# Kernel tuning notes

Hardware: AMD Instinct MI355X
Metric: run time of the kernel (lower is better)

Reference implementation:

```python
import jax, jax.numpy as jnp
import numpy as np

SIGMA = 0.248
PRNUM = 6
P = 7.5
K = 3.0
ALPHA = 2.5


def _gauss_kernel():
    # 5x5 normalized Gaussian, replicated per channel for depthwise conv [O=3,I=1,5,5]
    x = jnp.arange(-2, 3, dtype=jnp.float32)
    x2, y2 = jnp.meshgrid(x, x, indexing='xy')
    k = jnp.exp(-(x2 ** 2 + y2 ** 2) / (2.0 * SIGMA ** 2))
    k = k / jnp.sum(k)
    return jnp.broadcast_to(k[None, None], (3, 1, 5, 5))


def _dwconv(x, k):
    # x: [3,H,W]; depthwise 5x5 conv, padding=2 (matches F.conv2d(..., padding=2, groups=3))
    return jax.lax.conv_general_dilated(
        x[None], k, window_strides=(1, 1), padding=[(2, 2), (2, 2)],
        feature_group_count=3, dimension_numbers=('NCHW', 'OIHW', 'NCHW'))[0]


def _down2(x):
    # torch bilinear align_corners=False at exact scale 0.5 == 2x2 average pooling
    c, h, w = x.shape
    return x.reshape(c, h // 2, 2, w // 2, 2).mean(axis=(2, 4))


def _up(x, hw):
    # torch bilinear align_corners=False upsample (half-pixel centers) == jax linear resize
    return jax.image.resize(x, (x.shape[0], hw[0], hw[1]), method='linear')


def _foveate(img, fixs):
    C, H, W = img.shape
    k = _gauss_kernel()
    # build Gaussian pyramid
    G = img
    pyr = [G]
    for _ in range(1, PRNUM):
        G = _down2(_dwconv(G, k))
        pyr.append(G)
    # re-expand each level back to full res (interpolate then blur at each step)
    As = [pyr[0]]
    for i in range(1, PRNUM):
        cur = pyr[i]
        for j in range(i):
            hw = (cur.shape[1] * 2, cur.shape[2] * 2) if j < i - 1 else (H, W)
            cur = _dwconv(_up(cur, hw), k)
        As.append(cur)
    As = jnp.stack(As)  # [prNum, 3, H, W]

    # radial eccentricity map (min distance over fixations)
    x = jnp.arange(W, dtype=jnp.float32)
    y = jnp.arange(H, dtype=jnp.float32)
    x2d, y2d = jnp.meshgrid(x, y, indexing='xy')  # each [H, W]
    d = jnp.sqrt((x2d[None] - fixs[:, 0, None, None]) ** 2 +
                 (y2d[None] - fixs[:, 1, None, None]) ** 2) / P
    theta = jnp.min(d, axis=0)
    R = ALPHA / (theta + ALPHA)

    Ts = [jnp.exp(-((2.0 ** (i - 3)) * R / SIGMA) ** 2 * K) for i in range(1, PRNUM)]
    Ts.append(jnp.zeros_like(R))

    om = np.minimum(np.sqrt(np.log(2.0) / K) / (2.0 ** np.arange(-2, 3)) * SIGMA, 1.0)
    omega = np.concatenate([om, [0.0]]).astype(np.float32)  # [prNum]

    layer_ind = jnp.zeros_like(R)
    for i in range(1, PRNUM):
        ind = (R >= omega[i]) & (R <= omega[i - 1])
        layer_ind = jnp.where(ind, jnp.float32(i), layer_ind)

    Bs = [(0.5 - Ts[i]) / (Ts[i - 1] - Ts[i] + 1e-5) for i in range(1, PRNUM)]

    Ms = []
    for i in range(PRNUM):
        base = jnp.ones_like(R) if i == 0 else 1.0 - Bs[i - 1]
        M = jnp.where(layer_ind == i, base, jnp.float32(0.0))
        if i < PRNUM - 1:
            M = jnp.where(layer_ind == i + 1, Bs[i], M)
        Ms.append(M)
    Ms = jnp.stack(Ms)  # [prNum, H, W]

    # blend: sum_p Ms[p] * As[p, c]
    im_fov = jnp.einsum('phw,pchw->chw', Ms, As)
    return im_fov


def setup_inputs() -> dict:
    key = jax.random.key(0)
    k1, k2 = jax.random.split(key)
    img = jax.random.uniform(k1, (3, 2048, 2048), dtype=jnp.float32) * 255.0
    fixs = jax.random.uniform(k2, (4, 2), dtype=jnp.float32) * 2048.0
    return {'img': img, 'fixs': fixs}


def reference(img, fixs):
    return _foveate(img, fixs)
```

## Files before the change

### kernel.cpp

```cpp
#include <hip/hip_runtime.h>
#include <math.h>

#define HW2048 (2048ull*2048ull)
typedef float f4 __attribute__((ext_vector_type(4)));
typedef float f2 __attribute__((ext_vector_type(2)));
typedef _Float16 h8 __attribute__((ext_vector_type(8)));

struct BP {
  float P[4][3];
  float D2[5];
  float cc[5];
};

__global__ __launch_bounds__(256) void down12_k(const float* __restrict__ img,
                                                float* __restrict__ C1,
                                                float* __restrict__ p2) {
  int X = blockIdx.x * 16 + threadIdx.x;
  int Y = blockIdx.y * 16 + threadIdx.y;
  int c = blockIdx.z;
  const float* ip = img + (size_t)c * HW2048 + (size_t)(4 * Y) * 2048 + 4 * X;
  f4 r0 = __builtin_nontemporal_load((const f4*)(ip));
  f4 r1 = __builtin_nontemporal_load((const f4*)(ip + 2048));
  f4 r2 = __builtin_nontemporal_load((const f4*)(ip + 4096));
  f4 r3 = __builtin_nontemporal_load((const f4*)(ip + 6144));
  float a00 = 0.25f * (r0.x + r0.y + r1.x + r1.y);
  float a01 = 0.25f * (r0.z + r0.w + r1.z + r1.w);
  float a10 = 0.25f * (r2.x + r2.y + r3.x + r3.y);
  float a11 = 0.25f * (r2.z + r2.w + r3.z + r3.w);
  float* cp = C1 + (size_t)c * 1048576 + (size_t)(2 * Y) * 1024 + 2 * X;
  f2 u; u.x = a00; u.y = a01; *(f2*)cp = u;
  f2 v; v.x = a10; v.y = a11; *(f2*)(cp + 1024) = v;
  p2[((size_t)c * 512 + Y) * 512 + X] = 0.25f * (a00 + a01 + a10 + a11);
}

__global__ __launch_bounds__(256) void down345_k(const float* __restrict__ p2,
                                                 float* __restrict__ p3,
                                                 float* __restrict__ p4,
                                                 float* __restrict__ p5) {
  __shared__ float t4[16][17];
  int tx = threadIdx.x, ty = threadIdx.y;
  int X = blockIdx.x * 16 + tx;
  int Y = blockIdx.y * 16 + ty;
  int c = blockIdx.z;
  const float* ip = p2 + (size_t)c * 262144 + (size_t)(4 * Y) * 512 + 4 * X;
  f4 r0 = *(const f4*)(ip);
  f4 r1 = *(const f4*)(ip + 512);
  f4 r2 = *(const f4*)(ip + 1024);
  f4 r3 = *(const f4*)(ip + 1536);
  float a00 = 0.25f * (r0.x + r0.y + r1.x + r1.y);
  float a01 = 0.25f * (r0.z + r0.w + r1.z + r1.w);
  float a10 = 0.25f * (r2.x + r2.y + r3.x + r3.y);
  float a11 = 0.25f * (r2.z + r2.w + r3.z + r3.w);
  float* cp = p3 + (size_t)c * 65536 + (size_t)(2 * Y) * 256 + 2 * X;
  f2 u; u.x = a00; u.y = a01; *(f2*)cp = u;
  f2 v; v.x = a10; v.y = a11; *(f2*)(cp + 256) = v;
  float m = 0.25f * (a00 + a01 + a10 + a11);
  t4[ty][tx] = m;
  p4[((size_t)c * 128 + Y) * 128 + X] = m;
  __syncthreads();
  int tid = ty * 16 + tx;
  if (tid < 64) {
    int y = tid >> 3, x = tid & 7;
    float w = 0.25f * (t4[2*y][2*x] + t4[2*y][2*x+1] + t4[2*y+1][2*x] + t4[2*y+1][2*x+1]);
    p5[((size_t)c * 64 + blockIdx.y * 8 + y) * 64 + blockIdx.x * 8 + x] = w;
  }
}

__device__ __forceinline__ void up_coords(int o, int n, int& i0, int& i1, float& w0) {
  int m = o >> 1;
  if (o & 1) { i0 = m; i1 = min(m + 1, n - 1); w0 = 0.75f; }
  else       { i0 = max(m - 1, 0); i1 = m;     w0 = 0.25f; }
}

__global__ __launch_bounds__(256) void upchain_k(const float* __restrict__ p3,
                                                 const float* __restrict__ p4,
                                                 const float* __restrict__ p5,
                                                 float* __restrict__ U3,
                                                 float* __restrict__ U4,
                                                 float* __restrict__ U5) {
  __shared__ float a[19][20];
  __shared__ float mid[34][35];
  int z = blockIdx.z, im = z / 3, ch = z - im * 3;
  int X0 = blockIdx.x * 64, Y0 = blockIdx.y * 64;
  int tid = threadIdx.x;
  int bx1 = X0 / 4 - 1, by1 = Y0 / 4 - 1;
  int bx2 = X0 / 2 - 1, by2 = Y0 / 2 - 1;

  if (im == 2) {
    const float* s = p5 + ch * 4096;
    for (int j = tid; j < 18 * 18; j += 256) {
      int r = j / 18, cc = j % 18;
      int gy = min(max(by1 + r, 0), 127), gx = min(max(bx1 + cc, 0), 127);
      int r0, r1, c0, c1; float wy0, wx0;
      up_coords(gy, 64, r0, r1, wy0);
      up_coords(gx, 64, c0, c1, wx0);
      float wy1 = 1.f - wy0, wx1 = 1.f - wx0;
      a[r][cc] = wy0 * (wx0 * s[r0*64+c0] + wx1 * s[r0*64+c1])
               + wy1 * (wx0 * s[r1*64+c0] + wx1 * s[r1*64+c1]);
    }
    __syncthreads();
    for (int j = tid; j < 34 * 34; j += 256) {
      int r = j / 34, cc = j % 34;
      int gy = min(max(by2 + r, 0), 255), gx = min(max(bx2 + cc, 0), 255);
      int r0, r1, c0, c1; float wy0, wx0;
      up_coords(gy, 128, r0, r1, wy0);
      up_coords(gx, 128, c0, c1, wx0);
      float wy1 = 1.f - wy0, wx1 = 1.f - wx0;
      int a0 = r0 - by1, a1 = r1 - by1, b0 = c0 - bx1, b1 = c1 - bx1;
      mid[r][cc] = wy0 * (wx0 * a[a0][b0] + wx1 * a[a0][b1])
                 + wy1 * (wx0 * a[a1][b0] + wx1 * a[a1][b1]);
    }
    __syncthreads();
  } else if (im == 1) {
    const float* s = p4 + ch * 16384;
    for (int j = tid; j < 34 * 34; j += 256) {
      int r = j / 34, cc = j % 34;
      int gy = min(max(by2 + r, 0), 255), gx = min(max(bx2 + cc, 0), 255);
      int r0, r1, c0, c1; float wy0, wx0;
      up_coords(gy, 128, r0, r1, wy0);
      up_coords(gx, 128, c0, c1, wx0);
      float wy1 = 1.f - wy0, wx1 = 1.f - wx0;
      mid[r][cc] = wy0 * (wx0 * s[r0*128+c0] + wx1 * s[r0*128+c1])
                 + wy1 * (wx0 * s[r1*128+c0] + wx1 * s[r1*128+c1]);
    }
    __syncthreads();
  }

  float* dst = (im == 0) ? U3 : (im == 1) ? U4 : U5;
  const float* p3g = p3 + ch * 65536;
  int lx = tid & 63, lyb = tid >> 6;
#pragma unroll 4
  for (int rr = 0; rr < 16; ++rr) {
    int ly = lyb * 16 + rr;
    int x = X0 + lx, y = Y0 + ly;
    int r0, r1, c0, c1; float wy0, wx0;
    up_coords(y, 256, r0, r1, wy0);
    up_coords(x, 256, c0, c1, wx0);
    float wy1 = 1.f - wy0, wx1 = 1.f - wx0;
    float v;
    if (im == 0) {
      v = wy0 * (wx0 * p3g[r0*256+c0] + wx1 * p3g[r0*256+c1])
        + wy1 * (wx0 * p3g[r1*256+c0] + wx1 * p3g[r1*256+c1]);
    } else {
      int a0 = r0 - by2, a1 = r1 - by2, b0 = c0 - bx2, b1 = c1 - bx2;
      v = wy0 * (wx0 * mid[a0][b0] + wx1 * mid[a0][b1])
        + wy1 * (wx0 * mid[a1][b0] + wx1 * mid[a1][b1]);
    }
    dst[((size_t)ch * 512 + y) * 512 + x] = v;
  }
}

__device__ __forceinline__ float calc_B(float dd, int L, const BP& bp) {
  float d = sqrtf(dd);
  float R = 18.75f / (d + 18.75f);
  float R2 = R * R;
  float cL = (L == 1) ? bp.cc[1] : (L == 2) ? bp.cc[2] : (L == 3) ? bp.cc[3] : bp.cc[4];
  float cm = (L == 1) ? bp.cc[0] : (L == 2) ? bp.cc[1] : (L == 3) ? bp.cc[2] : (L == 4) ? bp.cc[3] : bp.cc[4];
  float tsL = (L >= 5) ? 0.f : __expf(-cL * R2);
  float tsm = __expf(-cm * R2);
  return (0.5f - tsL) / (tsm - tsL + 1e-5f);
}

__global__ __launch_bounds__(256) void classify_k(const float* __restrict__ fixs, int nf,
                                                  unsigned* __restrict__ meta,
                                                  h8* __restrict__ Bbuf, BP bp) {
  int xs = blockIdx.x * 64 + threadIdx.x;
  int yp = blockIdx.y * 4 + threadIdx.y;
  int x0 = xs * 4, y0 = yp * 2;
  int span = yp * 512 + xs;

  float d2[2][4];
#pragma unroll
  for (int j = 0; j < 2; ++j)
#pragma unroll
    for (int i = 0; i < 4; ++i) d2[j][i] = 3.4e38f;
  for (int f = 0; f < nf; ++f) {
    float dx0 = (float)x0 - fixs[2 * f], dy0 = (float)y0 - fixs[2 * f + 1];
#pragma unroll
    for (int j = 0; j < 2; ++j) {
      float dy = dy0 + (float)j, dy2 = dy * dy;
#pragma unroll
      for (int i = 0; i < 4; ++i) {
        float dx = dx0 + (float)i;
        d2[j][i] = fminf(d2[j][i], dx * dx + dy2);
      }
    }
  }

  unsigned m = 0;
  h8 b;
#pragma unroll
  for (int j = 0; j < 2; ++j)
#pragma unroll
    for (int i = 0; i < 4; ++i) {
      float dd = d2[j][i];
      int l = (dd >= bp.D2[0]) + (dd >= bp.D2[1]) + (dd >= bp.D2[2]) +
              (dd >= bp.D2[3]) + (dd >= bp.D2[4]);
      m |= (unsigned)l << (4 * (j * 4 + i));
      float B = (l == 0) ? 0.f : calc_B(dd, l, bp);
      b[j * 4 + i] = (_Float16)B;
    }
  meta[span] = m;
  Bbuf[span] = b;
}

__device__ __forceinline__ void s2c(const float* __restrict__ b, int x0, int y0,
                                    const BP& bp, float o[2][4]) {
  int t = x0 >> 2, ky = y0 >> 2, yph = y0 & 3;
  int c[3], r[3];
#pragma unroll
  for (int j = 0; j < 3; ++j) {
    c[j] = min(max(t - 1 + j, 0), 511);
    r[j] = min(max(ky - 1 + j, 0), 511);
  }
  float v[3][3];
#pragma unroll
  for (int j = 0; j < 3; ++j) {
    const float* row = b + r[j] * 512;
    v[j][0] = row[c[0]]; v[j][1] = row[c[1]]; v[j][2] = row[c[2]];
  }
  const float* wr0 = bp.P[yph];
  const float* wr1 = bp.P[yph + 1];
  float rv0[3], rv1[3];
#pragma unroll
  for (int i = 0; i < 3; ++i) {
    rv0[i] = wr0[0] * v[0][i] + wr0[1] * v[1][i] + wr0[2] * v[2][i];
    rv1[i] = wr1[0] * v[0][i] + wr1[1] * v[1][i] + wr1[2] * v[2][i];
  }
#pragma unroll
  for (int p = 0; p < 4; ++p) {
    o[0][p] = bp.P[p][0] * rv0[0] + bp.P[p][1] * rv0[1] + bp.P[p][2] * rv0[2];
    o[1][p] = bp.P[p][0] * rv1[0] + bp.P[p][1] * rv1[1] + bp.P[p][2] * rv1[2];
  }
}

__device__ __forceinline__ void s1c(const float* __restrict__ b, int x0, int y0,
                                    float o[2][4]) {
  int q0 = x0 >> 1, qy = y0 >> 1;
  int c[4], r[3];
#pragma unroll
  for (int i = 0; i < 4; ++i) c[i] = min(max(q0 - 1 + i, 0), 1023);
#pragma unroll
  for (int j = 0; j < 3; ++j) r[j] = min(max(qy - 1 + j, 0), 1023);
  float v[3][4];
#pragma unroll
  for (int j = 0; j < 3; ++j) {
    const float* row = b + r[j] * 1024;
    v[j][0] = row[c[0]]; v[j][1] = row[c[1]]; v[j][2] = row[c[2]]; v[j][3] = row[c[3]];
  }
  float rv0[4], rv1[4];
#pragma unroll
  for (int i = 0; i < 4; ++i) {
    rv0[i] = 0.25f * v[0][i] + 0.75f * v[1][i];
    rv1[i] = 0.75f * v[1][i] + 0.25f * v[2][i];
  }
  o[0][0] = 0.25f * rv0[0] + 0.75f * rv0[1];
  o[0][1] = 0.75f * rv0[1] + 0.25f * rv0[2];
  o[0][2] = 0.25f * rv0[1] + 0.75f * rv0[2];
  o[0][3] = 0.75f * rv0[2] + 0.25f * rv0[3];
  o[1][0] = 0.25f * rv1[0] + 0.75f * rv1[1];
  o[1][1] = 0.75f * rv1[1] + 0.25f * rv1[2];
  o[1][2] = 0.25f * rv1[1] + 0.75f * rv1[2];
  o[1][3] = 0.75f * rv1[2] + 0.25f * rv1[3];
}

__device__ __forceinline__ void sample_level(int l, int x0, int y0,
    const float* __restrict__ imgc, const float* __restrict__ C1c,
    const float* __restrict__ b2, const float* __restrict__ b3,
    const float* __restrict__ b4, const float* __restrict__ b5,
    const BP& bp, float o[2][4]) {
  if (l == 0) {
    f4 v0 = *(const f4*)(imgc + (size_t)y0 * 2048 + x0);
    f4 v1 = *(const f4*)(imgc + (size_t)(y0 + 1) * 2048 + x0);
    o[0][0] = v0.x; o[0][1] = v0.y; o[0][2] = v0.z; o[0][3] = v0.w;
    o[1][0] = v1.x; o[1][1] = v1.y; o[1][2] = v1.z; o[1][3] = v1.w;
  } else if (l == 1) {
    s1c(C1c, x0, y0, o);
  } else {
    const float* b = (l == 2) ? b2 : (l == 3) ? b3 : (l == 4) ? b4 : b5;
    s2c(b, x0, y0, bp, o);
  }
}

__global__ __launch_bounds__(256) void blendc_k(
    const float* __restrict__ img, const float* __restrict__ C1,
    const float* __restrict__ B2, const float* __restrict__ B3,
    const float* __restrict__ B4, const float* __restrict__ B5,
    const unsigned* __restrict__ meta, const h8* __restrict__ Bbuf,
    float* __restrict__ out, BP bp) {
  int xs = blockIdx.x * 64 + threadIdx.x;
  int yp = blockIdx.y * 4 + threadIdx.y;
  int ch = blockIdx.z;
  int x0 = xs * 4, y0 = yp * 2;
  int span = yp * 512 + xs;
  size_t ob = (size_t)ch * HW2048 + (size_t)y0 * 2048 + x0;
  const float* imgc = img + (size_t)ch * HW2048;

  unsigned m = meta[span];

  if (m == 0u) {
    f4 v0 = *(const f4*)(imgc + (size_t)y0 * 2048 + x0);
    f4 v1 = *(const f4*)(imgc + (size_t)(y0 + 1) * 2048 + x0);
    __builtin_nontemporal_store(v0, (f4*)(out + ob));
    __builtin_nontemporal_store(v1, (f4*)(out + ob + 2048));
    return;
  }

  h8 bh = Bbuf[span];
  const float* C1c = C1 + (size_t)ch * 1048576;
  const float* b2 = B2 + (size_t)ch * 262144;
  const float* b3 = B3 + (size_t)ch * 262144;
  const float* b4 = B4 + (size_t)ch * 262144;
  const float* b5 = B5 + (size_t)ch * 262144;

  unsigned lmin = 15u, lmax = 0u;
#pragma unroll
  for (int k = 0; k < 8; ++k) {
    unsigned l = (m >> (4 * k)) & 15u;
    lmin = min(lmin, l);
    lmax = max(lmax, l);
  }

  float sA[2][4];
  float sB[2][4];
  float sC[2][4];
  sample_level((int)lmax,     x0, y0, imgc, C1c, b2, b3, b4, b5, bp, sA);
  sample_level((int)lmax - 1, x0, y0, imgc, C1c, b2, b3, b4, b5, bp, sB);
#pragma unroll
  for (int j = 0; j < 2; ++j)
#pragma unroll
    for (int i = 0; i < 4; ++i) sC[j][i] = sB[j][i];
  if (lmin != lmax && lmax >= 2u)
    sample_level((int)lmax - 2, x0, y0, imgc, C1c, b2, b3, b4, b5, bp, sC);

  float res[2][4];
#pragma unroll
  for (int j = 0; j < 2; ++j)
#pragma unroll
    for (int i = 0; i < 4; ++i) {
      int k = j * 4 + i;
      unsigned l = (m >> (4 * k)) & 15u;
      float B = (float)bh[k];
      bool top = (l == lmax);
      float hi = top ? sA[j][i] : sB[j][i];
      float lo = top ? sB[j][i] : sC[j][i];
      res[j][i] = B * lo + (1.f - B) * hi;
    }

  f4 v0, v1;
  v0.x = res[0][0]; v0.y = res[0][1]; v0.z = res[0][2]; v0.w = res[0][3];
  v1.x = res[1][0]; v1.y = res[1][1]; v1.z = res[1][2]; v1.w = res[1][3];
  __builtin_nontemporal_store(v0, (f4*)(out + ob));
  __builtin_nontemporal_store(v1, (f4*)(out + ob + 2048));
}

extern "C" void kernel_launch(void* const* d_in, const int* in_sizes, int n_in,
                              void* d_out, int out_size, void* d_ws, size_t ws_size,
                              hipStream_t stream) {
  const float* img  = (const float*)d_in[0];
  const float* fixs = (const float*)d_in[1];
  int nf = in_sizes[1] / 2;
  float* out = (float*)d_out;
  float* ws  = (float*)d_ws;

  BP bp;
  const double sig = 0.248, Kd = 3.0, Pd = 7.5, Ad = 2.5;
  double obv = sqrt(log(2.0) / Kd) * sig;
  for (int j = 0; j < 5; ++j) {
    double om = obv * pow(2.0, 2 - j);
    double Dj = Pd * Ad * (1.0 / om - 1.0);
    bp.D2[j] = (float)(Dj * Dj);
  }
  for (int X = 0; X < 5; ++X)
    bp.cc[X] = (float)(Kd * pow(2.0, 2.0 * (X - 2)) / (sig * sig));
  const float Pt[4][3] = {{0.375f, 0.625f, 0.f},
                          {0.1875f, 0.75f, 0.0625f},
                          {0.0625f, 0.75f, 0.1875f},
                          {0.f, 0.625f, 0.375f}};
  for (int a = 0; a < 4; ++a) for (int t = 0; t < 3; ++t) bp.P[a][t] = Pt[a][t];

  size_t o = 0;
  float* C1 = ws + o; o += 3ull * 1024 * 1024;
  float* p2 = ws + o; o += 3ull * 512 * 512;
  float* p3 = ws + o; o += 3ull * 256 * 256;
  float* p4 = ws + o; o += 3ull * 128 * 128;
  float* p5 = ws + o; o += 3ull * 64 * 64;
  float* U3 = ws + o; o += 3ull * 512 * 512;
  float* U4 = ws + o; o += 3ull * 512 * 512;
  float* U5 = ws + o; o += 3ull * 512 * 512;
  unsigned* meta = (unsigned*)(ws + o); o += 512ull * 1024;
  h8* Bbuf = (h8*)(ws + o); o += 4ull * 512 * 1024;

  down12_k  <<<dim3(32, 32, 3), dim3(16, 16), 0, stream>>>(img, C1, p2);
  down345_k <<<dim3(8, 8, 3),   dim3(16, 16), 0, stream>>>(p2, p3, p4, p5);
  upchain_k <<<dim3(8, 8, 9),   dim3(256),    0, stream>>>(p3, p4, p5, U3, U4, U5);
  classify_k<<<dim3(8, 256),    dim3(64, 4),  0, stream>>>(fixs, nf, meta, Bbuf, bp);
  blendc_k  <<<dim3(8, 256, 3), dim3(64, 4),  0, stream>>>(img, C1, p2, U3, U4, U5,
                                                           meta, Bbuf, out, bp);
}
```

Before: 140.9 us.

## Fuse classification into blend kernel and loop over channels per thread

Removes the separate classify kernel and its meta/half-precision B buffers. The blend kernel now computes the fixation distances, level bounds and blend weights itself, once per pixel group, and then loops over the three channels inside each thread instead of using a z-dimension grid. This drops one launch plus the global write and read of per-pixel metadata, and shares the weight computation across channels. In exchange the grid has a third as many threads, each doing more serial work, which lowers parallelism and latency hiding. B is now kept in fp32 rather than fp16.

```diff
diff --git a/kernel.cpp b/kernel.cpp
--- a/kernel.cpp
+++ b/kernel.cpp
@@ -4,7 +4,6 @@
 #define HW2048 (2048ull*2048ull)
 typedef float f4 __attribute__((ext_vector_type(4)));
 typedef float f2 __attribute__((ext_vector_type(2)));
-typedef _Float16 h8 __attribute__((ext_vector_type(8)));
 
 struct BP {
   float P[4][3];
@@ -150,60 +149,6 @@
   }
 }
 
-__device__ __forceinline__ float calc_B(float dd, int L, const BP& bp) {
-  float d = sqrtf(dd);
-  float R = 18.75f / (d + 18.75f);
-  float R2 = R * R;
-  float cL = (L == 1) ? bp.cc[1] : (L == 2) ? bp.cc[2] : (L == 3) ? bp.cc[3] : bp.cc[4];
-  float cm = (L == 1) ? bp.cc[0] : (L == 2) ? bp.cc[1] : (L == 3) ? bp.cc[2] : (L == 4) ? bp.cc[3] : bp.cc[4];
-  float tsL = (L >= 5) ? 0.f : __expf(-cL * R2);
-  float tsm = __expf(-cm * R2);
-  return (0.5f - tsL) / (tsm - tsL + 1e-5f);
-}
-
-__global__ __launch_bounds__(256) void classify_k(const float* __restrict__ fixs, int nf,
-                                                  unsigned* __restrict__ meta,
-                                                  h8* __restrict__ Bbuf, BP bp) {
-  int xs = blockIdx.x * 64 + threadIdx.x;
-  int yp = blockIdx.y * 4 + threadIdx.y;
-  int x0 = xs * 4, y0 = yp * 2;
-  int span = yp * 512 + xs;
-
-  float d2[2][4];
-#pragma unroll
-  for (int j = 0; j < 2; ++j)
-#pragma unroll
-    for (int i = 0; i < 4; ++i) d2[j][i] = 3.4e38f;
-  for (int f = 0; f < nf; ++f) {
-    float dx0 = (float)x0 - fixs[2 * f], dy0 = (float)y0 - fixs[2 * f + 1];
-#pragma unroll
-    for (int j = 0; j < 2; ++j) {
-      float dy = dy0 + (float)j, dy2 = dy * dy;
-#pragma unroll
-      for (int i = 0; i < 4; ++i) {
-        float dx = dx0 + (float)i;
-        d2[j][i] = fminf(d2[j][i], dx * dx + dy2);
-      }
-    }
-  }
-
-  unsigned m = 0;
-  h8 b;
-#pragma unroll
-  for (int j = 0; j < 2; ++j)
-#pragma unroll
-    for (int i = 0; i < 4; ++i) {
-      float dd = d2[j][i];
-      int l = (dd >= bp.D2[0]) + (dd >= bp.D2[1]) + (dd >= bp.D2[2]) +
-              (dd >= bp.D2[3]) + (dd >= bp.D2[4]);
-      m |= (unsigned)l << (4 * (j * 4 + i));
-      float B = (l == 0) ? 0.f : calc_B(dd, l, bp);
-      b[j * 4 + i] = (_Float16)B;
-    }
-  meta[span] = m;
-  Bbuf[span] = b;
-}
-
 __device__ __forceinline__ void s2c(const float* __restrict__ b, int x0, int y0,
                                     const BP& bp, float o[2][4]) {
   int t = x0 >> 2, ky = y0 >> 2, yph = y0 & 3;
@@ -282,76 +227,133 @@
   }
 }
 
-__global__ __launch_bounds__(256) void blendc_k(
+__global__ __launch_bounds__(256) void fblend_k(
     const float* __restrict__ img, const float* __restrict__ C1,
     const float* __restrict__ B2, const float* __restrict__ B3,
     const float* __restrict__ B4, const float* __restrict__ B5,
-    const unsigned* __restrict__ meta, const h8* __restrict__ Bbuf,
+    const float* __restrict__ fixs, int nf,
     float* __restrict__ out, BP bp) {
   int xs = blockIdx.x * 64 + threadIdx.x;
   int yp = blockIdx.y * 4 + threadIdx.y;
-  int ch = blockIdx.z;
   int x0 = xs * 4, y0 = yp * 2;
-  int span = yp * 512 + xs;
-  size_t ob = (size_t)ch * HW2048 + (size_t)y0 * 2048 + x0;
-  const float* imgc = img + (size_t)ch * HW2048;
-
-  unsigned m = meta[span];
-
-  if (m == 0u) {
-    f4 v0 = *(const f4*)(imgc + (size_t)y0 * 2048 + x0);
-    f4 v1 = *(const f4*)(imgc + (size_t)(y0 + 1) * 2048 + x0);
-    __builtin_nontemporal_store(v0, (f4*)(out + ob));
-    __builtin_nontemporal_store(v1, (f4*)(out + ob + 2048));
+  size_t ob0 = (size_t)y0 * 2048 + x0;
+
+  float d2[2][4];
+#pragma unroll
+  for (int j = 0; j < 2; ++j)
+#pragma unroll
+    for (int i = 0; i < 4; ++i) d2[j][i] = 3.4e38f;
+  for (int f = 0; f < nf; ++f) {
+    float dx0 = (float)x0 - fixs[2 * f], dy0 = (float)y0 - fixs[2 * f + 1];
+#pragma unroll
+    for (int j = 0; j < 2; ++j) {
+      float dy = dy0 + (float)j, dy2 = dy * dy;
+#pragma unroll
+      for (int i = 0; i < 4; ++i) {
+        float dx = dx0 + (float)i;
+        d2[j][i] = fminf(d2[j][i], dx * dx + dy2);
+      }
+    }
+  }
+
+  float dmn = d2[0][0], dmx = d2[0][0];
+#pragma unroll
+  for (int j = 0; j < 2; ++j)
+#pragma unroll
+    for (int i = 0; i < 4; ++i) {
+      dmn = fminf(dmn, d2[j][i]);
+      dmx = fmaxf(dmx, d2[j][i]);
+    }
+  int lmax = (dmx >= bp.D2[0]) + (dmx >= bp.D2[1]) + (dmx >= bp.D2[2]) +
+             (dmx >= bp.D2[3]) + (dmx >= bp.D2[4]);
+
+  if (lmax == 0) {
+#pragma unroll
+    for (int ch = 0; ch < 3; ++ch) {
+      const float* imgc = img + (size_t)ch * HW2048;
+      f4 v0 = *(const f4*)(imgc + ob0);
+      f4 v1 = *(const f4*)(imgc + ob0 + 2048);
+      __builtin_nontemporal_store(v0, (f4*)(out + (size_t)ch * HW2048 + ob0));
+      __builtin_nontemporal_store(v1, (f4*)(out + (size_t)ch * HW2048 + ob0 + 2048));
+    }
     return;
   }
 
-  h8 bh = Bbuf[span];
-  const float* C1c = C1 + (size_t)ch * 1048576;
-  const float* b2 = B2 + (size_t)ch * 262144;
-  const float* b3 = B3 + (size_t)ch * 262144;
-  const float* b4 = B4 + (size_t)ch * 262144;
-  const float* b5 = B5 + (size_t)ch * 262144;
-
-  unsigned lmin = 15u, lmax = 0u;
-#pragma unroll
-  for (int k = 0; k < 8; ++k) {
-    unsigned l = (m >> (4 * k)) & 15u;
-    lmin = min(lmin, l);
-    lmax = max(lmax, l);
-  }
-
-  float sA[2][4];
-  float sB[2][4];
-  float sC[2][4];
-  sample_level((int)lmax,     x0, y0, imgc, C1c, b2, b3, b4, b5, bp, sA);
-  sample_level((int)lmax - 1, x0, y0, imgc, C1c, b2, b3, b4, b5, bp, sB);
+  int lmin = (dmn >= bp.D2[0]) + (dmn >= bp.D2[1]) + (dmn >= bp.D2[2]) +
+             (dmn >= bp.D2[3]) + (dmn >= bp.D2[4]);
+  bool mixed = (lmin != lmax);
+
+  float thr  = (lmax == 1) ? bp.D2[0] : (lmax == 2) ? bp.D2[1] :
+               (lmax == 3) ? bp.D2[2] : (lmax == 4) ? bp.D2[3] : bp.D2[4];
+  float cL_A = (lmax <= 4) ? ((lmax == 1) ? bp.cc[1] : (lmax == 2) ? bp.cc[2] :
+               (lmax == 3) ? bp.cc[3] : bp.cc[4]) : bp.cc[4];
+  float cm_A = (lmax == 1) ? bp.cc[0] : (lmax == 2) ? bp.cc[1] :
+               (lmax == 3) ? bp.cc[2] : (lmax == 4) ? bp.cc[3] : bp.cc[4];
+  float cL_B = cm_A;
+  float cm_B = (lmax <= 2) ? bp.cc[0] : (lmax == 3) ? bp.cc[1] :
+               (lmax == 4) ? bp.cc[2] : bp.cc[3];
+  bool tsL_A_zero = (lmax >= 5);
+
+  float Bv[2][4];
+  bool  tp[2][4];
 #pragma unroll
   for (int j = 0; j < 2; ++j)
 #pragma unroll
-    for (int i = 0; i < 4; ++i) sC[j][i] = sB[j][i];
-  if (lmin != lmax && lmax >= 2u)
-    sample_level((int)lmax - 2, x0, y0, imgc, C1c, b2, b3, b4, b5, bp, sC);
-
-  float res[2][4];
-#pragma unroll
-  for (int j = 0; j < 2; ++j)
-#pragma unroll
     for (int i = 0; i < 4; ++i) {
-      int k = j * 4 + i;
-      unsigned l = (m >> (4 * k)) & 15u;
-      float B = (float)bh[k];
-      bool top = (l == lmax);
-      float hi = top ? sA[j][i] : sB[j][i];
-      float lo = top ? sB[j][i] : sC[j][i];
-      res[j][i] = B * lo + (1.f - B) * hi;
-    }
-
-  f4 v0, v1;
-  v0.x = res[0][0]; v0.y = res[0][1]; v0.z = res[0][2]; v0.w = res[0][3];
-  v1.x = res[1][0]; v1.y = res[1][1]; v1.z = res[1][2]; v1.w = res[1][3];
-  __builtin_nontemporal_store(v0, (f4*)(out + ob));
-  __builtin_nontemporal_store(v1, (f4*)(out + ob + 2048));
+      float dd = d2[j][i];
+      bool top = (dd >= thr);
+      tp[j][i] = top;
+      float d = sqrtf(dd);
+      float R = 18.75f / (d + 18.75f);
+      float R2 = R * R;
+      float cL = top ? cL_A : cL_B;
+      float cm = top ? cm_A : cm_B;
+      float tsL = (top && tsL_A_zero) ? 0.f : __expf(-cL * R2);
+      float tsm = __expf(-cm * R2);
+      float B = (0.5f - tsL) / (tsm - tsL + 1e-5f);
+      if (!top && lmax == 1) B = 0.f;
+      Bv[j][i] = B;
+    }
+
+#pragma unroll
+  for (int ch = 0; ch < 3; ++ch) {
+    const float* imgc = img + (size_t)ch * HW2048;
+    const float* C1c  = C1 + (size_t)ch * 1048576;
+    const float* b2   = B2 + (size_t)ch * 262144;
+    const float* b3   = B3 + (size_t)ch * 262144;
+    const float* b4   = B4 + (size_t)ch * 262144;
+    const float* b5   = B5 + (size_t)ch * 262144;
+
+    float sA[2][4];
+    float sB[2][4];
+    float sC[2][4];
+    sample_level(lmax,     x0, y0, imgc, C1c, b2, b3, b4, b5, bp, sA);
+    sample_level(lmax - 1, x0, y0, imgc, C1c, b2, b3, b4, b5, bp, sB);
+#pragma unroll
+    for (int j = 0; j < 2; ++j)
+#pragma unroll
+      for (int i = 0; i < 4; ++i) sC[j][i] = sB[j][i];
+    if (mixed && lmax >= 2)
+      sample_level(lmax - 2, x0, y0, imgc, C1c, b2, b3, b4, b5, bp, sC);
+
+    float res[2][4];
+#pragma unroll
+    for (int j = 0; j < 2; ++j)
+#pragma unroll
+      for (int i = 0; i < 4; ++i) {
+        float B = Bv[j][i];
+        bool top = tp[j][i];
+        float hi = top ? sA[j][i] : sB[j][i];
+        float lo = top ? sB[j][i] : sC[j][i];
+        res[j][i] = B * lo + (1.f - B) * hi;
+      }
+
+    f4 v0, v1;
+    v0.x = res[0][0]; v0.y = res[0][1]; v0.z = res[0][2]; v0.w = res[0][3];
+    v1.x = res[1][0]; v1.y = res[1][1]; v1.z = res[1][2]; v1.w = res[1][3];
+    __builtin_nontemporal_store(v0, (f4*)(out + (size_t)ch * HW2048 + ob0));
+    __builtin_nontemporal_store(v1, (f4*)(out + (size_t)ch * HW2048 + ob0 + 2048));
+  }
 }
 
 extern "C" void kernel_launch(void* const* d_in, const int* in_sizes, int n_in,
@@ -388,13 +390,10 @@
   float* U3 = ws + o; o += 3ull * 512 * 512;
   float* U4 = ws + o; o += 3ull * 512 * 512;
   float* U5 = ws + o; o += 3ull * 512 * 512;
-  unsigned* meta = (unsigned*)(ws + o); o += 512ull * 1024;
-  h8* Bbuf = (h8*)(ws + o); o += 4ull * 512 * 1024;
 
   down12_k  <<<dim3(32, 32, 3), dim3(16, 16), 0, stream>>>(img, C1, p2);
   down345_k <<<dim3(8, 8, 3),   dim3(16, 16), 0, stream>>>(p2, p3, p4, p5);
   upchain_k <<<dim3(8, 8, 9),   dim3(256),    0, stream>>>(p3, p4, p5, U3, U4, U5);
-  classify_k<<<dim3(8, 256),    dim3(64, 4),  0, stream>>>(fixs, nf, meta, Bbuf, bp);
-  blendc_k  <<<dim3(8, 256, 3), dim3(64, 4),  0, stream>>>(img, C1, p2, U3, U4, U5,
-                                                           meta, Bbuf, out, bp);
-}
+  fblend_k  <<<dim3(8, 256),    dim3(64, 4),  0, stream>>>(img, C1, p2, U3, U4, U5,
+                                                           fixs, nf, out, bp);
+}
```

After: 134.9 us. 1.04x faster.
